# Kernel optimization log

Hardware: AMD Instinct MI355X
Metric: run time of the kernel (lower is better)

Reference implementation:

```python
import jax, jax.numpy as jnp
import numpy as np

N, DIM = 20000, 2
E2, E3 = 150000, 100000
H = 512
IN_PAIR = 2 * DIM + 2    # arity*dim + arity (sigma repeated per object)
IN_TRIPLE = 3 * DIM + 3


def _lin(k, fan_in, fan_out):
    return jax.random.normal(k, (fan_in, fan_out), jnp.float32) / np.sqrt(fan_in)


def setup_inputs() -> dict:
    key = jax.random.key(0)
    ks = jax.random.split(key, 18)
    inp = {
        "x": jax.random.normal(ks[0], (N, DIM), jnp.float32),
        "sigma": jax.random.uniform(ks[1], (1,), jnp.float32) + 0.1,
        "edges_pair": jax.random.randint(ks[2], (E2, 2), 0, N),
        "edges_triple": jax.random.randint(ks[3], (E3, 3), 0, N),
        # per-relation-type TimeInputEnergyMLP params (2 hidden layers + scalar head)
        "pW1": _lin(ks[4], IN_PAIR, H), "pb1": jnp.zeros((H,), jnp.float32),
        "pW2": _lin(ks[5], H, H),       "pb2": jnp.zeros((H,), jnp.float32),
        "pW3": _lin(ks[6], H, 1),       "pb3": jnp.zeros((1,), jnp.float32),
        "tW1": _lin(ks[7], IN_TRIPLE, H), "tb1": jnp.zeros((H,), jnp.float32),
        "tW2": _lin(ks[8], H, H),         "tb2": jnp.zeros((H,), jnp.float32),
        "tW3": _lin(ks[9], H, 1),         "tb3": jnp.zeros((1,), jnp.float32),
    }
    return inp


def _mlp_energy(h, W1, b1, W2, b2, W3, b3):
    # h: (E, in_dim) -> (E, 1) scalar energy per edge
    h = jax.nn.silu(h @ W1 + b1)
    h = jax.nn.silu(h @ W2 + b2)
    return h @ W3 + b3


def reference(x, sigma, edges_pair, edges_triple,
              pW1, pb1, pW2, pb2, pW3, pb3,
              tW1, tb1, tW2, tb2, tW3, tb3):
    def total_energy(xx):
        # pair edges: gather -> (E2, 2*DIM), sigma repeated per object -> (E2, 2)
        xp = xx[edges_pair].reshape(edges_pair.shape[0], -1)
        sp = jnp.broadcast_to(sigma, (edges_pair.shape[0], 2))
        ep = _mlp_energy(jnp.concatenate([xp, sp], axis=-1),
                         pW1, pb1, pW2, pb2, pW3, pb3).sum()
        # triple edges
        xt = xx[edges_triple].reshape(edges_triple.shape[0], -1)
        st = jnp.broadcast_to(sigma, (edges_triple.shape[0], 3))
        et = _mlp_energy(jnp.concatenate([xt, st], axis=-1),
                         tW1, tb1, tW2, tb2, tW3, tb3).sum()
        return ep + et

    energy, grad = jax.value_and_grad(total_energy)(x)
    return energy, grad
```

## Files before the change

kernel.cpp:

```cpp
#include <hip/hip_runtime.h>
#include <hip/hip_bf16.h>

#define HDIM 512
#define TILE 64
#define TPB 512

typedef __attribute__((ext_vector_type(8))) short short8;
typedef __attribute__((ext_vector_type(4))) short s16x4;
typedef __attribute__((ext_vector_type(4))) float f32x4;

__device__ __forceinline__ unsigned short f2bf(float x) {
  __hip_bfloat16 h = __float2bfloat16(x);
  return *reinterpret_cast<unsigned short*>(&h);
}
__device__ __forceinline__ float bf2f(unsigned short h) {
  return __uint_as_float(((unsigned)h) << 16);
}
__device__ __forceinline__ float fsig(float z) {
  return __builtin_amdgcn_rcpf(1.f + __expf(-z));
}
__device__ __forceinline__ int bidx(int e, int n) {
  return e * HDIM + (n ^ ((e & 15) << 3));
}

__global__ void prep_weights(const float* __restrict__ pW2, const float* __restrict__ tW2,
                             unsigned short* __restrict__ pWf, unsigned short* __restrict__ pWb,
                             unsigned short* __restrict__ tWf, unsigned short* __restrict__ tWb) {
  int i = blockIdx.x * blockDim.x + threadIdx.x;
  if (i >= HDIM * HDIM) return;
  int j  = i & 7;
  int l  = (i >> 3) & 63;
  int kb = (i >> 9) & 15;
  int nb = i >> 13;
  int kpos = kb * 32 + ((l >> 4) << 3) + j;
  int npos = nb * 16 + (l & 15);
  pWf[i] = f2bf(pW2[kpos * HDIM + npos]);
  pWb[i] = f2bf(pW2[npos * HDIM + kpos]);
  tWf[i] = f2bf(tW2[kpos * HDIM + npos]);
  tWb[i] = f2bf(tW2[npos * HDIM + kpos]);
}

__global__ void prep_w1(const float* __restrict__ W1, int IN, int GD,
                        unsigned short* __restrict__ hi, unsigned short* __restrict__ lo,
                        unsigned short* __restrict__ p5) {
  int i = blockIdx.x * blockDim.x + threadIdx.x;
  if (i < 32 * 64 * 8) {
    int j = i & 7, l = (i >> 3) & 63, nb = i >> 9;
    int k = ((l >> 4) << 3) + j;
    int col = nb * 16 + (l & 15);
    float v = (k < IN) ? W1[k * HDIM + col] : 0.f;
    unsigned short h = f2bf(v);
    hi[i] = h;
    lo[i] = f2bf(v - bf2f(h));
  } else if (i < 32 * 64 * 8 + 16 * 64 * 8) {
    int i2 = i - 32 * 64 * 8;
    int j = i2 & 7, l = (i2 >> 3) & 63, kk = i2 >> 9;
    int lm = l & 15, q = l >> 4;
    int k = kk * 32 + q * 8 + j;
    p5[i2] = f2bf((lm < GD) ? W1[lm * HDIM + k] : 0.f);
  }
}

__global__ void __launch_bounds__(TPB, 2)
energy_kernel(const float* __restrict__ x, const float* __restrict__ sigp,
              const int* __restrict__ ep, const int* __restrict__ et,
              int E2, int E3, int nb2,
              const unsigned short* __restrict__ pW1hi, const unsigned short* __restrict__ pW1lo,
              const unsigned short* __restrict__ pW1p5,
              const unsigned short* __restrict__ tW1hi, const unsigned short* __restrict__ tW1lo,
              const unsigned short* __restrict__ tW1p5,
              const float* __restrict__ pb1, const float* __restrict__ tb1,
              const unsigned short* __restrict__ pWf, const unsigned short* __restrict__ pWb,
              const unsigned short* __restrict__ tWf, const unsigned short* __restrict__ tWb,
              const float* __restrict__ pb2, const float* __restrict__ tb2,
              const float* __restrict__ pw3, const float* __restrict__ tw3,
              const float* __restrict__ pb3, const float* __restrict__ tb3,
              float* __restrict__ out) {
  __shared__ __align__(16) unsigned short bufA[TILE * HDIM];
  __shared__ __align__(16) float h0s[TILE][16];
  __shared__ float dh0sT[8][TILE];
  __shared__ int   idxs[TILE * 3];
  __shared__ float blockE;

  const bool isP = (int)blockIdx.x < nb2;
  const int arity = isP ? 2 : 3;
  const int GD = 2 * arity;
  const int Etot = isP ? E2 : E3;
  const int* __restrict__ edges = isP ? ep : et;
  const unsigned short* __restrict__ W1hi = isP ? pW1hi : tW1hi;
  const unsigned short* __restrict__ W1lo = isP ? pW1lo : tW1lo;
  const unsigned short* __restrict__ W1p5 = isP ? pW1p5 : tW1p5;
  const unsigned short* __restrict__ Wf = isP ? pWf : tWf;
  const unsigned short* __restrict__ Wb = isP ? pWb : tWb;
  const float* __restrict__ b1 = isP ? pb1 : tb1;
  const float* __restrict__ b2 = isP ? pb2 : tb2;
  const float* __restrict__ w3 = isP ? pw3 : tw3;
  const float* __restrict__ b3p = isP ? pb3 : tb3;

  const int tid  = threadIdx.x;
  const int lane = tid & 63;
  const int w    = tid >> 6;
  const int q    = lane >> 4;
  const int lm   = lane & 15;
  const int tile0 = (isP ? (int)blockIdx.x : (int)blockIdx.x - nb2) * TILE;
  const int vcnt  = min(TILE, Etot - tile0);
  const float sigma = sigp[0];

  if (tid == 0) blockE = 0.f;
  ((float*)dh0sT)[tid] = 0.f;
  if (tid < TILE * arity) {
    int e = tid / arity;
    idxs[tid] = (e < vcnt) ? edges[(size_t)tile0 * arity + tid] : 0;
  }
  __syncthreads();
  if (tid < TILE) {
#pragma unroll
    for (int k = 0; k < 16; ++k) h0s[tid][k] = 0.f;
    if (tid < vcnt) {
      for (int o = 0; o < arity; ++o) {
        int id = idxs[tid * arity + o];
        h0s[tid][o * 2 + 0] = x[id * 2 + 0];
        h0s[tid][o * 2 + 1] = x[id * 2 + 1];
        h0s[tid][arity * 2 + o] = sigma;
      }
    }
  }
  __syncthreads();

  const int n0 = w * 64;

  short8 Hh[4], Hl[4];
#pragma unroll
  for (int ef = 0; ef < 4; ++ef) {
    f32x4 v0 = {0.f, 0.f, 0.f, 0.f}, v1 = {0.f, 0.f, 0.f, 0.f};
    if (q < 2) {
      const float* p = &h0s[ef * 16 + lm][q * 8];
      v0 = *(const f32x4*)p;
      v1 = *(const f32x4*)(p + 4);
    }
#pragma unroll
    for (int j = 0; j < 4; ++j) {
      unsigned short ha = f2bf(v0[j]);
      Hh[ef][j] = (short)ha;
      Hl[ef][j] = (short)f2bf(v0[j] - bf2f(ha));
      unsigned short hb = f2bf(v1[j]);
      Hh[ef][j + 4] = (short)hb;
      Hl[ef][j + 4] = (short)f2bf(v1[j] - bf2f(hb));
    }
  }

  f32x4 acc[4][4];
#pragma unroll
  for (int mf = 0; mf < 4; ++mf)
#pragma unroll
    for (int ef = 0; ef < 4; ++ef) acc[mf][ef] = (f32x4){0.f, 0.f, 0.f, 0.f};

#pragma unroll
  for (int mf = 0; mf < 4; ++mf) {
    short8 A1h = *(const short8*)(W1hi + (((w * 4 + mf) * 64 + lane) << 3));
    short8 A1l = *(const short8*)(W1lo + (((w * 4 + mf) * 64 + lane) << 3));
#pragma unroll
    for (int ef = 0; ef < 4; ++ef) {
      acc[mf][ef] = __builtin_amdgcn_mfma_f32_16x16x32_bf16(A1h, Hh[ef], acc[mf][ef], 0, 0, 0);
      acc[mf][ef] = __builtin_amdgcn_mfma_f32_16x16x32_bf16(A1l, Hh[ef], acc[mf][ef], 0, 0, 0);
      acc[mf][ef] = __builtin_amdgcn_mfma_f32_16x16x32_bf16(A1h, Hl[ef], acc[mf][ef], 0, 0, 0);
    }
  }
#pragma unroll
  for (int mf = 0; mf < 4; ++mf) {
    f32x4 b1x = *(const f32x4*)&b1[n0 + mf * 16 + q * 4];
#pragma unroll
    for (int ef = 0; ef < 4; ++ef) {
      bool val = (ef * 16 + lm) < vcnt;
      s16x4 pk;
#pragma unroll
      for (int r = 0; r < 4; ++r) {
        float z = acc[mf][ef][r] + b1x[r];
        float s = fsig(z);
        pk[r] = (short)f2bf(val ? z * s : 0.f);
      }
      *(s16x4*)&bufA[bidx(ef * 16 + lm, n0 + mf * 16 + q * 4)] = pk;
    }
  }
  __syncthreads();

#pragma unroll
  for (int mf = 0; mf < 4; ++mf)
#pragma unroll
    for (int ef = 0; ef < 4; ++ef) acc[mf][ef] = (f32x4){0.f, 0.f, 0.f, 0.f};

  {
    short8 af_cur[4];
#pragma unroll
    for (int mf = 0; mf < 4; ++mf)
      af_cur[mf] = *(const short8*)(Wf + ((((w * 4 + mf) * 16 + 0) * 64 + lane) << 3));
#pragma unroll
    for (int kk = 0; kk < 16; ++kk) {
      short8 af_nxt[4];
      int kn = (kk + 1) & 15;
#pragma unroll
      for (int mf = 0; mf < 4; ++mf)
        af_nxt[mf] = *(const short8*)(Wf + ((((w * 4 + mf) * 16 + kn) * 64 + lane) << 3));
      short8 hb[4];
#pragma unroll
      for (int ef = 0; ef < 4; ++ef)
        hb[ef] = *(const short8*)&bufA[bidx(ef * 16 + lm, kk * 32 + q * 8)];
      __builtin_amdgcn_s_setprio(1);
#pragma unroll
      for (int mf = 0; mf < 4; ++mf)
#pragma unroll
        for (int ef = 0; ef < 4; ++ef)
          acc[mf][ef] = __builtin_amdgcn_mfma_f32_16x16x32_bf16(af_cur[mf], hb[ef], acc[mf][ef], 0, 0, 0);
      __builtin_amdgcn_s_setprio(0);
#pragma unroll
      for (int mf = 0; mf < 4; ++mf) af_cur[mf] = af_nxt[mf];
    }
  }

  float epart = 0.f;
#pragma unroll
  for (int mf = 0; mf < 4; ++mf) {
    f32x4 b2x = *(const f32x4*)&b2[n0 + mf * 16 + q * 4];
    f32x4 w3x = *(const f32x4*)&w3[n0 + mf * 16 + q * 4];
#pragma unroll
    for (int ef = 0; ef < 4; ++ef) {
      bool val = (ef * 16 + lm) < vcnt;
#pragma unroll
      for (int r = 0; r < 4; ++r) {
        float z = acc[mf][ef][r] + b2x[r];
        float s = fsig(z);
        float h2 = z * s;
        float sp = s * (1.f + z * (1.f - s));
        epart += val ? h2 * w3x[r] : 0.f;
        acc[mf][ef][r] = val ? w3x[r] * sp : 0.f;
      }
    }
  }

  __syncthreads();
#pragma unroll
  for (int mf = 0; mf < 4; ++mf)
#pragma unroll
    for (int ef = 0; ef < 4; ++ef) {
      s16x4 pk;
#pragma unroll
      for (int r = 0; r < 4; ++r) pk[r] = (short)f2bf(acc[mf][ef][r]);
      *(s16x4*)&bufA[bidx(ef * 16 + lm, n0 + mf * 16 + q * 4)] = pk;
    }
#pragma unroll
  for (int off = 32; off > 0; off >>= 1) epart += __shfl_down(epart, off, 64);
  if (lane == 0) atomicAdd(&blockE, epart);
  __syncthreads();
  if (tid == 0) atomicAdd(out, blockE + (float)vcnt * b3p[0]);

#pragma unroll
  for (int mf = 0; mf < 4; ++mf)
#pragma unroll
    for (int ef = 0; ef < 4; ++ef) acc[mf][ef] = (f32x4){0.f, 0.f, 0.f, 0.f};

  {
    short8 af_cur[4];
#pragma unroll
    for (int mf = 0; mf < 4; ++mf)
      af_cur[mf] = *(const short8*)(Wb + ((((w * 4 + mf) * 16 + 0) * 64 + lane) << 3));
#pragma unroll
    for (int kk = 0; kk < 16; ++kk) {
      short8 af_nxt[4];
      int kn = (kk + 1) & 15;
#pragma unroll
      for (int mf = 0; mf < 4; ++mf)
        af_nxt[mf] = *(const short8*)(Wb + ((((w * 4 + mf) * 16 + kn) * 64 + lane) << 3));
      short8 hb[4];
#pragma unroll
      for (int ef = 0; ef < 4; ++ef)
        hb[ef] = *(const short8*)&bufA[bidx(ef * 16 + lm, kk * 32 + q * 8)];
      __builtin_amdgcn_s_setprio(1);
#pragma unroll
      for (int mf = 0; mf < 4; ++mf)
#pragma unroll
        for (int ef = 0; ef < 4; ++ef)
          acc[mf][ef] = __builtin_amdgcn_mfma_f32_16x16x32_bf16(af_cur[mf], hb[ef], acc[mf][ef], 0, 0, 0);
      __builtin_amdgcn_s_setprio(0);
#pragma unroll
      for (int mf = 0; mf < 4; ++mf) af_cur[mf] = af_nxt[mf];
    }
  }

#pragma unroll
  for (int mf = 0; mf < 4; ++mf) {
    short8 A1h = *(const short8*)(W1hi + (((w * 4 + mf) * 64 + lane) << 3));
    f32x4 zacc[4];
#pragma unroll
    for (int ef = 0; ef < 4; ++ef) zacc[ef] = (f32x4){0.f, 0.f, 0.f, 0.f};
#pragma unroll
    for (int ef = 0; ef < 4; ++ef)
      zacc[ef] = __builtin_amdgcn_mfma_f32_16x16x32_bf16(A1h, Hh[ef], zacc[ef], 0, 0, 0);
    f32x4 b1x = *(const f32x4*)&b1[n0 + mf * 16 + q * 4];
#pragma unroll
    for (int ef = 0; ef < 4; ++ef)
#pragma unroll
      for (int r = 0; r < 4; ++r) {
        float z = zacc[ef][r] + b1x[r];
        float s = fsig(z);
        float sp = s * (1.f + z * (1.f - s));
        acc[mf][ef][r] *= sp;
      }
  }
  __syncthreads();
#pragma unroll
  for (int mf = 0; mf < 4; ++mf)
#pragma unroll
    for (int ef = 0; ef < 4; ++ef) {
      s16x4 pk;
#pragma unroll
      for (int r = 0; r < 4; ++r) pk[r] = (short)f2bf(acc[mf][ef][r]);
      *(s16x4*)&bufA[bidx(ef * 16 + lm, n0 + mf * 16 + q * 4)] = pk;
    }
  __syncthreads();

  {
    f32x4 pacc[4];
#pragma unroll
    for (int ef = 0; ef < 4; ++ef) pacc[ef] = (f32x4){0.f, 0.f, 0.f, 0.f};
#pragma unroll
    for (int t = 0; t < 2; ++t) {
      int kk = w * 2 + t;
      short8 a5 = *(const short8*)(W1p5 + ((kk * 64 + lane) << 3));
      short8 db[4];
#pragma unroll
      for (int ef = 0; ef < 4; ++ef)
        db[ef] = *(const short8*)&bufA[bidx(ef * 16 + lm, kk * 32 + q * 8)];
#pragma unroll
      for (int ef = 0; ef < 4; ++ef)
        pacc[ef] = __builtin_amdgcn_mfma_f32_16x16x32_bf16(a5, db[ef], pacc[ef], 0, 0, 0);
    }
#pragma unroll
    for (int ef = 0; ef < 4; ++ef)
#pragma unroll
      for (int r = 0; r < 4; ++r) {
        int g = q * 4 + r;
        if (g < GD) atomicAdd(&dh0sT[g][ef * 16 + lm], pacc[ef][r]);
      }
  }
  __syncthreads();

  {
    int e = tid & 63, g = tid >> 6;
    if (e < vcnt && g < GD) {
      int obj = g >> 1, d = g & 1;
      atomicAdd(&out[1 + idxs[e * arity + obj] * 2 + d], dh0sT[g][e]);
    }
  }
}

extern "C" void kernel_launch(void* const* d_in, const int* in_sizes, int n_in,
                              void* d_out, int out_size, void* d_ws, size_t ws_size,
                              hipStream_t stream) {
  const float* x    = (const float*)d_in[0];
  const float* sig  = (const float*)d_in[1];
  const int*   ep   = (const int*)d_in[2];
  const int*   et   = (const int*)d_in[3];
  const float* pW1  = (const float*)d_in[4];
  const float* pb1  = (const float*)d_in[5];
  const float* pW2  = (const float*)d_in[6];
  const float* pb2  = (const float*)d_in[7];
  const float* pW3  = (const float*)d_in[8];
  const float* pb3  = (const float*)d_in[9];
  const float* tW1  = (const float*)d_in[10];
  const float* tb1  = (const float*)d_in[11];
  const float* tW2  = (const float*)d_in[12];
  const float* tb2  = (const float*)d_in[13];
  const float* tW3  = (const float*)d_in[14];
  const float* tb3  = (const float*)d_in[15];
  const int E2 = in_sizes[2] / 2;
  const int E3 = in_sizes[3] / 3;
  float* out = (float*)d_out;

  unsigned short* pWf = (unsigned short*)d_ws;
  unsigned short* pWb = pWf + HDIM * HDIM;
  unsigned short* tWf = pWb + HDIM * HDIM;
  unsigned short* tWb = tWf + HDIM * HDIM;
  unsigned short* pW1hi = tWb + HDIM * HDIM;
  unsigned short* pW1lo = pW1hi + 32 * 64 * 8;
  unsigned short* pW1p5 = pW1lo + 32 * 64 * 8;
  unsigned short* tW1hi = pW1p5 + 16 * 64 * 8;
  unsigned short* tW1lo = tW1hi + 32 * 64 * 8;
  unsigned short* tW1p5 = tW1lo + 32 * 64 * 8;

  const int nb2 = (E2 + TILE - 1) / TILE;
  const int nb3 = (E3 + TILE - 1) / TILE;

  hipMemsetAsync(d_out, 0, (size_t)out_size * sizeof(float), stream);
  prep_weights<<<(HDIM * HDIM + 255) / 256, 256, 0, stream>>>(pW2, tW2, pWf, pWb, tWf, tWb);
  prep_w1<<<(32 * 64 * 8 + 16 * 64 * 8 + 255) / 256, 256, 0, stream>>>(pW1, 6, 4, pW1hi, pW1lo, pW1p5);
  prep_w1<<<(32 * 64 * 8 + 16 * 64 * 8 + 255) / 256, 256, 0, stream>>>(tW1, 9, 6, tW1hi, tW1lo, tW1p5);
  energy_kernel<<<nb2 + nb3, TPB, 0, stream>>>(
      x, sig, ep, et, E2, E3, nb2,
      pW1hi, pW1lo, pW1p5, tW1hi, tW1lo, tW1p5, pb1, tb1,
      pWf, pWb, tWf, tWb, pb2, tb2, pW3, tW3, pb3, tb3, out);
}
```

Before: 437.3 us.

## Switch MFMA tiling from 16x16x32 to 32x32x16 bf16 instructions

Reworks every matrix stage of the fused energy/gradient kernel (layer-1 split-precision product, forward and backward 512x512 layers, input-gradient projection) to use 32x32x16 MFMA tiles instead of 16x16x32. Weight pre-swizzle kernels and workspace offsets are re-laid out to match the new fragment layout. Larger MFMA tiles mean fewer instructions and more operand reuse per LDS and global fragment load. The cost is more accumulator registers per wave (four f32x16 instead of sixteen f32x4 blocks is the same count, but the epilogue indexing changes) and possible LDS bank-conflict differences under the existing swizzle.

```diff
diff --git a/kernel.cpp b/kernel.cpp
--- a/kernel.cpp
+++ b/kernel.cpp
@@ -8,6 +8,7 @@
 typedef __attribute__((ext_vector_type(8))) short short8;
 typedef __attribute__((ext_vector_type(4))) short s16x4;
 typedef __attribute__((ext_vector_type(4))) float f32x4;
+typedef __attribute__((ext_vector_type(16))) float f32x16;
 
 __device__ __forceinline__ unsigned short f2bf(float x) {
   __hip_bfloat16 h = __float2bfloat16(x);
@@ -30,10 +31,10 @@
   if (i >= HDIM * HDIM) return;
   int j  = i & 7;
   int l  = (i >> 3) & 63;
-  int kb = (i >> 9) & 15;
-  int nb = i >> 13;
-  int kpos = kb * 32 + ((l >> 4) << 3) + j;
-  int npos = nb * 16 + (l & 15);
+  int kc = (i >> 9) & 31;
+  int nb = i >> 14;
+  int npos = nb * 32 + (l & 31);
+  int kpos = kc * 16 + ((l >> 5) << 3) + j;
   pWf[i] = f2bf(pW2[kpos * HDIM + npos]);
   pWb[i] = f2bf(pW2[npos * HDIM + kpos]);
   tWf[i] = f2bf(tW2[kpos * HDIM + npos]);
@@ -44,20 +45,20 @@
                         unsigned short* __restrict__ hi, unsigned short* __restrict__ lo,
                         unsigned short* __restrict__ p5) {
   int i = blockIdx.x * blockDim.x + threadIdx.x;
-  if (i < 32 * 64 * 8) {
+  if (i < 16 * 64 * 8) {
     int j = i & 7, l = (i >> 3) & 63, nb = i >> 9;
-    int k = ((l >> 4) << 3) + j;
-    int col = nb * 16 + (l & 15);
+    int k = ((l >> 5) << 3) + j;
+    int col = nb * 32 + (l & 31);
     float v = (k < IN) ? W1[k * HDIM + col] : 0.f;
     unsigned short h = f2bf(v);
     hi[i] = h;
     lo[i] = f2bf(v - bf2f(h));
-  } else if (i < 32 * 64 * 8 + 16 * 64 * 8) {
-    int i2 = i - 32 * 64 * 8;
-    int j = i2 & 7, l = (i2 >> 3) & 63, kk = i2 >> 9;
-    int lm = l & 15, q = l >> 4;
-    int k = kk * 32 + q * 8 + j;
-    p5[i2] = f2bf((lm < GD) ? W1[lm * HDIM + k] : 0.f);
+  } else if (i < 16 * 64 * 8 + 32 * 64 * 8) {
+    int i2 = i - 16 * 64 * 8;
+    int j = i2 & 7, l = (i2 >> 3) & 63, kc = i2 >> 9;
+    int g = l & 31;
+    int n = kc * 16 + ((l >> 5) << 3) + j;
+    p5[i2] = f2bf((g < GD) ? W1[g * HDIM + n] : 0.f);
   }
 }
 
@@ -100,8 +101,8 @@
   const int tid  = threadIdx.x;
   const int lane = tid & 63;
   const int w    = tid >> 6;
-  const int q    = lane >> 4;
-  const int lm   = lane & 15;
+  const int l31  = lane & 31;
+  const int lh   = lane >> 5;
   const int tile0 = (isP ? (int)blockIdx.x : (int)blockIdx.x - nb2) * TILE;
   const int vcnt  = min(TILE, Etot - tile0);
   const float sigma = sigp[0];
@@ -129,124 +130,155 @@
 
   const int n0 = w * 64;
 
-  short8 Hh[4], Hl[4];
-#pragma unroll
-  for (int ef = 0; ef < 4; ++ef) {
-    f32x4 v0 = {0.f, 0.f, 0.f, 0.f}, v1 = {0.f, 0.f, 0.f, 0.f};
-    if (q < 2) {
-      const float* p = &h0s[ef * 16 + lm][q * 8];
-      v0 = *(const f32x4*)p;
-      v1 = *(const f32x4*)(p + 4);
-    }
-#pragma unroll
-    for (int j = 0; j < 4; ++j) {
-      unsigned short ha = f2bf(v0[j]);
-      Hh[ef][j] = (short)ha;
-      Hl[ef][j] = (short)f2bf(v0[j] - bf2f(ha));
-      unsigned short hb = f2bf(v1[j]);
-      Hh[ef][j + 4] = (short)hb;
-      Hl[ef][j + 4] = (short)f2bf(v1[j] - bf2f(hb));
-    }
-  }
-
-  f32x4 acc[4][4];
-#pragma unroll
-  for (int mf = 0; mf < 4; ++mf)
-#pragma unroll
-    for (int ef = 0; ef < 4; ++ef) acc[mf][ef] = (f32x4){0.f, 0.f, 0.f, 0.f};
-
-#pragma unroll
-  for (int mf = 0; mf < 4; ++mf) {
-    short8 A1h = *(const short8*)(W1hi + (((w * 4 + mf) * 64 + lane) << 3));
-    short8 A1l = *(const short8*)(W1lo + (((w * 4 + mf) * 64 + lane) << 3));
-#pragma unroll
-    for (int ef = 0; ef < 4; ++ef) {
-      acc[mf][ef] = __builtin_amdgcn_mfma_f32_16x16x32_bf16(A1h, Hh[ef], acc[mf][ef], 0, 0, 0);
-      acc[mf][ef] = __builtin_amdgcn_mfma_f32_16x16x32_bf16(A1l, Hh[ef], acc[mf][ef], 0, 0, 0);
-      acc[mf][ef] = __builtin_amdgcn_mfma_f32_16x16x32_bf16(A1h, Hl[ef], acc[mf][ef], 0, 0, 0);
-    }
-  }
-#pragma unroll
-  for (int mf = 0; mf < 4; ++mf) {
-    f32x4 b1x = *(const f32x4*)&b1[n0 + mf * 16 + q * 4];
-#pragma unroll
-    for (int ef = 0; ef < 4; ++ef) {
-      bool val = (ef * 16 + lm) < vcnt;
-      s16x4 pk;
-#pragma unroll
-      for (int r = 0; r < 4; ++r) {
-        float z = acc[mf][ef][r] + b1x[r];
-        float s = fsig(z);
-        pk[r] = (short)f2bf(val ? z * s : 0.f);
-      }
-      *(s16x4*)&bufA[bidx(ef * 16 + lm, n0 + mf * 16 + q * 4)] = pk;
-    }
-  }
-  __syncthreads();
-
-#pragma unroll
-  for (int mf = 0; mf < 4; ++mf)
-#pragma unroll
-    for (int ef = 0; ef < 4; ++ef) acc[mf][ef] = (f32x4){0.f, 0.f, 0.f, 0.f};
-
+  short8 Hh[2];
+  f32x16 acc[2][2];
   {
-    short8 af_cur[4];
-#pragma unroll
-    for (int mf = 0; mf < 4; ++mf)
-      af_cur[mf] = *(const short8*)(Wf + ((((w * 4 + mf) * 16 + 0) * 64 + lane) << 3));
-#pragma unroll
-    for (int kk = 0; kk < 16; ++kk) {
-      short8 af_nxt[4];
-      int kn = (kk + 1) & 15;
-#pragma unroll
-      for (int mf = 0; mf < 4; ++mf)
-        af_nxt[mf] = *(const short8*)(Wf + ((((w * 4 + mf) * 16 + kn) * 64 + lane) << 3));
-      short8 hb[4];
-#pragma unroll
-      for (int ef = 0; ef < 4; ++ef)
-        hb[ef] = *(const short8*)&bufA[bidx(ef * 16 + lm, kk * 32 + q * 8)];
+    short8 Hl[2];
+#pragma unroll
+    for (int eb = 0; eb < 2; ++eb) {
+      const float* p = &h0s[eb * 32 + l31][lh * 8];
+      f32x4 v0 = *(const f32x4*)p;
+      f32x4 v1 = *(const f32x4*)(p + 4);
+#pragma unroll
+      for (int j = 0; j < 4; ++j) {
+        unsigned short ha = f2bf(v0[j]);
+        Hh[eb][j] = (short)ha;
+        Hl[eb][j] = (short)f2bf(v0[j] - bf2f(ha));
+        unsigned short hb_ = f2bf(v1[j]);
+        Hh[eb][j + 4] = (short)hb_;
+        Hl[eb][j + 4] = (short)f2bf(v1[j] - bf2f(hb_));
+      }
+    }
+#pragma unroll
+    for (int nb = 0; nb < 2; ++nb)
+#pragma unroll
+      for (int eb = 0; eb < 2; ++eb)
+#pragma unroll
+        for (int r = 0; r < 16; ++r) acc[nb][eb][r] = 0.f;
+
+#pragma unroll
+    for (int nb = 0; nb < 2; ++nb) {
+      int nbg = w * 2 + nb;
+      short8 A1h = *(const short8*)(W1hi + ((nbg * 64 + lane) << 3));
+      short8 A1l = *(const short8*)(W1lo + ((nbg * 64 + lane) << 3));
+#pragma unroll
+      for (int eb = 0; eb < 2; ++eb) {
+        acc[nb][eb] = __builtin_amdgcn_mfma_f32_32x32x16_bf16(A1h, Hh[eb], acc[nb][eb], 0, 0, 0);
+        acc[nb][eb] = __builtin_amdgcn_mfma_f32_32x32x16_bf16(A1l, Hh[eb], acc[nb][eb], 0, 0, 0);
+        acc[nb][eb] = __builtin_amdgcn_mfma_f32_32x32x16_bf16(A1h, Hl[eb], acc[nb][eb], 0, 0, 0);
+      }
+    }
+  }
+#pragma unroll
+  for (int nb = 0; nb < 2; ++nb) {
+    int nbase = n0 + nb * 32;
+#pragma unroll
+    for (int eb = 0; eb < 2; ++eb) {
+      int e = eb * 32 + l31;
+      bool val = e < vcnt;
+#pragma unroll
+      for (int g = 0; g < 4; ++g) {
+        int n4 = nbase + 8 * g + 4 * lh;
+        f32x4 b1x = *(const f32x4*)&b1[n4];
+        s16x4 pk;
+#pragma unroll
+        for (int r = 0; r < 4; ++r) {
+          float z = acc[nb][eb][4 * g + r] + b1x[r];
+          float s = fsig(z);
+          pk[r] = (short)f2bf(val ? z * s : 0.f);
+        }
+        *(s16x4*)&bufA[bidx(e, n4)] = pk;
+      }
+    }
+  }
+  __syncthreads();
+
+#pragma unroll
+  for (int nb = 0; nb < 2; ++nb)
+#pragma unroll
+    for (int eb = 0; eb < 2; ++eb)
+#pragma unroll
+      for (int r = 0; r < 16; ++r) acc[nb][eb][r] = 0.f;
+
+  {
+    short8 af_cur[2][2];
+#pragma unroll
+    for (int nb = 0; nb < 2; ++nb)
+#pragma unroll
+      for (int t = 0; t < 2; ++t)
+        af_cur[nb][t] = *(const short8*)(Wf + ((((w * 2 + nb) * 32 + t) * 64 + lane) << 3));
+#pragma unroll
+    for (int c = 0; c < 16; ++c) {
+      short8 af_nxt[2][2];
+      int cn = (c + 1) & 15;
+#pragma unroll
+      for (int nb = 0; nb < 2; ++nb)
+#pragma unroll
+        for (int t = 0; t < 2; ++t)
+          af_nxt[nb][t] = *(const short8*)(Wf + ((((w * 2 + nb) * 32 + cn * 2 + t) * 64 + lane) << 3));
+      short8 hb[2][2];
+#pragma unroll
+      for (int eb = 0; eb < 2; ++eb)
+#pragma unroll
+        for (int t = 0; t < 2; ++t)
+          hb[eb][t] = *(const short8*)&bufA[bidx(eb * 32 + l31, (c * 2 + t) * 16 + lh * 8)];
       __builtin_amdgcn_s_setprio(1);
 #pragma unroll
-      for (int mf = 0; mf < 4; ++mf)
-#pragma unroll
-        for (int ef = 0; ef < 4; ++ef)
-          acc[mf][ef] = __builtin_amdgcn_mfma_f32_16x16x32_bf16(af_cur[mf], hb[ef], acc[mf][ef], 0, 0, 0);
+      for (int t = 0; t < 2; ++t)
+#pragma unroll
+        for (int nb = 0; nb < 2; ++nb)
+#pragma unroll
+          for (int eb = 0; eb < 2; ++eb)
+            acc[nb][eb] = __builtin_amdgcn_mfma_f32_32x32x16_bf16(af_cur[nb][t], hb[eb][t], acc[nb][eb], 0, 0, 0);
       __builtin_amdgcn_s_setprio(0);
 #pragma unroll
-      for (int mf = 0; mf < 4; ++mf) af_cur[mf] = af_nxt[mf];
+      for (int nb = 0; nb < 2; ++nb)
+#pragma unroll
+        for (int t = 0; t < 2; ++t) af_cur[nb][t] = af_nxt[nb][t];
     }
   }
 
   float epart = 0.f;
 #pragma unroll
-  for (int mf = 0; mf < 4; ++mf) {
-    f32x4 b2x = *(const f32x4*)&b2[n0 + mf * 16 + q * 4];
-    f32x4 w3x = *(const f32x4*)&w3[n0 + mf * 16 + q * 4];
-#pragma unroll
-    for (int ef = 0; ef < 4; ++ef) {
-      bool val = (ef * 16 + lm) < vcnt;
-#pragma unroll
-      for (int r = 0; r < 4; ++r) {
-        float z = acc[mf][ef][r] + b2x[r];
-        float s = fsig(z);
-        float h2 = z * s;
-        float sp = s * (1.f + z * (1.f - s));
-        epart += val ? h2 * w3x[r] : 0.f;
-        acc[mf][ef][r] = val ? w3x[r] * sp : 0.f;
-      }
-    }
-  }
-
-  __syncthreads();
-#pragma unroll
-  for (int mf = 0; mf < 4; ++mf)
-#pragma unroll
-    for (int ef = 0; ef < 4; ++ef) {
-      s16x4 pk;
-#pragma unroll
-      for (int r = 0; r < 4; ++r) pk[r] = (short)f2bf(acc[mf][ef][r]);
-      *(s16x4*)&bufA[bidx(ef * 16 + lm, n0 + mf * 16 + q * 4)] = pk;
-    }
+  for (int nb = 0; nb < 2; ++nb) {
+    int nbase = n0 + nb * 32;
+#pragma unroll
+    for (int eb = 0; eb < 2; ++eb) {
+      bool val = (eb * 32 + l31) < vcnt;
+#pragma unroll
+      for (int g = 0; g < 4; ++g) {
+        int n4 = nbase + 8 * g + 4 * lh;
+        f32x4 b2x = *(const f32x4*)&b2[n4];
+        f32x4 w3x = *(const f32x4*)&w3[n4];
+#pragma unroll
+        for (int r = 0; r < 4; ++r) {
+          float z = acc[nb][eb][4 * g + r] + b2x[r];
+          float s = fsig(z);
+          float h2 = z * s;
+          float sp = s * (1.f + z * (1.f - s));
+          epart += val ? h2 * w3x[r] : 0.f;
+          acc[nb][eb][4 * g + r] = val ? w3x[r] * sp : 0.f;
+        }
+      }
+    }
+  }
+
+  __syncthreads();
+#pragma unroll
+  for (int nb = 0; nb < 2; ++nb) {
+    int nbase = n0 + nb * 32;
+#pragma unroll
+    for (int eb = 0; eb < 2; ++eb) {
+      int e = eb * 32 + l31;
+#pragma unroll
+      for (int g = 0; g < 4; ++g) {
+        s16x4 pk;
+#pragma unroll
+        for (int r = 0; r < 4; ++r) pk[r] = (short)f2bf(acc[nb][eb][4 * g + r]);
+        *(s16x4*)&bufA[bidx(e, nbase + 8 * g + 4 * lh)] = pk;
+      }
+    }
+  }
 #pragma unroll
   for (int off = 32; off > 0; off >>= 1) epart += __shfl_down(epart, off, 64);
   if (lane == 0) atomicAdd(&blockE, epart);
@@ -254,92 +286,114 @@
   if (tid == 0) atomicAdd(out, blockE + (float)vcnt * b3p[0]);
 
 #pragma unroll
-  for (int mf = 0; mf < 4; ++mf)
-#pragma unroll
-    for (int ef = 0; ef < 4; ++ef) acc[mf][ef] = (f32x4){0.f, 0.f, 0.f, 0.f};
+  for (int nb = 0; nb < 2; ++nb)
+#pragma unroll
+    for (int eb = 0; eb < 2; ++eb)
+#pragma unroll
+      for (int r = 0; r < 16; ++r) acc[nb][eb][r] = 0.f;
 
   {
-    short8 af_cur[4];
-#pragma unroll
-    for (int mf = 0; mf < 4; ++mf)
-      af_cur[mf] = *(const short8*)(Wb + ((((w * 4 + mf) * 16 + 0) * 64 + lane) << 3));
-#pragma unroll
-    for (int kk = 0; kk < 16; ++kk) {
-      short8 af_nxt[4];
-      int kn = (kk + 1) & 15;
-#pragma unroll
-      for (int mf = 0; mf < 4; ++mf)
-        af_nxt[mf] = *(const short8*)(Wb + ((((w * 4 + mf) * 16 + kn) * 64 + lane) << 3));
-      short8 hb[4];
-#pragma unroll
-      for (int ef = 0; ef < 4; ++ef)
-        hb[ef] = *(const short8*)&bufA[bidx(ef * 16 + lm, kk * 32 + q * 8)];
+    short8 af_cur[2][2];
+#pragma unroll
+    for (int nb = 0; nb < 2; ++nb)
+#pragma unroll
+      for (int t = 0; t < 2; ++t)
+        af_cur[nb][t] = *(const short8*)(Wb + ((((w * 2 + nb) * 32 + t) * 64 + lane) << 3));
+#pragma unroll
+    for (int c = 0; c < 16; ++c) {
+      short8 af_nxt[2][2];
+      int cn = (c + 1) & 15;
+#pragma unroll
+      for (int nb = 0; nb < 2; ++nb)
+#pragma unroll
+        for (int t = 0; t < 2; ++t)
+          af_nxt[nb][t] = *(const short8*)(Wb + ((((w * 2 + nb) * 32 + cn * 2 + t) * 64 + lane) << 3));
+      short8 hb[2][2];
+#pragma unroll
+      for (int eb = 0; eb < 2; ++eb)
+#pragma unroll
+        for (int t = 0; t < 2; ++t)
+          hb[eb][t] = *(const short8*)&bufA[bidx(eb * 32 + l31, (c * 2 + t) * 16 + lh * 8)];
       __builtin_amdgcn_s_setprio(1);
 #pragma unroll
-      for (int mf = 0; mf < 4; ++mf)
-#pragma unroll
-        for (int ef = 0; ef < 4; ++ef)
-          acc[mf][ef] = __builtin_amdgcn_mfma_f32_16x16x32_bf16(af_cur[mf], hb[ef], acc[mf][ef], 0, 0, 0);
+      for (int t = 0; t < 2; ++t)
+#pragma unroll
+        for (int nb = 0; nb < 2; ++nb)
+#pragma unroll
+          for (int eb = 0; eb < 2; ++eb)
+            acc[nb][eb] = __builtin_amdgcn_mfma_f32_32x32x16_bf16(af_cur[nb][t], hb[eb][t], acc[nb][eb], 0, 0, 0);
       __builtin_amdgcn_s_setprio(0);
 #pragma unroll
-      for (int mf = 0; mf < 4; ++mf) af_cur[mf] = af_nxt[mf];
-    }
-  }
-
-#pragma unroll
-  for (int mf = 0; mf < 4; ++mf) {
-    short8 A1h = *(const short8*)(W1hi + (((w * 4 + mf) * 64 + lane) << 3));
-    f32x4 zacc[4];
-#pragma unroll
-    for (int ef = 0; ef < 4; ++ef) zacc[ef] = (f32x4){0.f, 0.f, 0.f, 0.f};
-#pragma unroll
-    for (int ef = 0; ef < 4; ++ef)
-      zacc[ef] = __builtin_amdgcn_mfma_f32_16x16x32_bf16(A1h, Hh[ef], zacc[ef], 0, 0, 0);
-    f32x4 b1x = *(const f32x4*)&b1[n0 + mf * 16 + q * 4];
-#pragma unroll
-    for (int ef = 0; ef < 4; ++ef)
+      for (int nb = 0; nb < 2; ++nb)
+#pragma unroll
+        for (int t = 0; t < 2; ++t) af_cur[nb][t] = af_nxt[nb][t];
+    }
+  }
+
+#pragma unroll
+  for (int nb = 0; nb < 2; ++nb) {
+    int nbg = w * 2 + nb;
+    int nbase = n0 + nb * 32;
+    short8 A1h = *(const short8*)(W1hi + ((nbg * 64 + lane) << 3));
+#pragma unroll
+    for (int eb = 0; eb < 2; ++eb) {
+      f32x16 zacc;
+#pragma unroll
+      for (int r = 0; r < 16; ++r) zacc[r] = 0.f;
+      zacc = __builtin_amdgcn_mfma_f32_32x32x16_bf16(A1h, Hh[eb], zacc, 0, 0, 0);
+#pragma unroll
+      for (int g = 0; g < 4; ++g) {
+        f32x4 b1x = *(const f32x4*)&b1[nbase + 8 * g + 4 * lh];
+#pragma unroll
+        for (int r = 0; r < 4; ++r) {
+          float z = zacc[4 * g + r] + b1x[r];
+          float s = fsig(z);
+          float sp = s * (1.f + z * (1.f - s));
+          acc[nb][eb][4 * g + r] *= sp;
+        }
+      }
+    }
+  }
+  __syncthreads();
+#pragma unroll
+  for (int nb = 0; nb < 2; ++nb) {
+    int nbase = n0 + nb * 32;
+#pragma unroll
+    for (int eb = 0; eb < 2; ++eb) {
+      int e = eb * 32 + l31;
+#pragma unroll
+      for (int g = 0; g < 4; ++g) {
+        s16x4 pk;
+#pragma unroll
+        for (int r = 0; r < 4; ++r) pk[r] = (short)f2bf(acc[nb][eb][4 * g + r]);
+        *(s16x4*)&bufA[bidx(e, nbase + 8 * g + 4 * lh)] = pk;
+      }
+    }
+  }
+  __syncthreads();
+
+  {
+    f32x16 pacc[2];
+#pragma unroll
+    for (int eb = 0; eb < 2; ++eb)
+#pragma unroll
+      for (int r = 0; r < 16; ++r) pacc[eb][r] = 0.f;
+#pragma unroll
+    for (int t = 0; t < 4; ++t) {
+      int kc = w * 4 + t;
+      short8 a5 = *(const short8*)(W1p5 + ((kc * 64 + lane) << 3));
+#pragma unroll
+      for (int eb = 0; eb < 2; ++eb) {
+        short8 db = *(const short8*)&bufA[bidx(eb * 32 + l31, kc * 16 + lh * 8)];
+        pacc[eb] = __builtin_amdgcn_mfma_f32_32x32x16_bf16(a5, db, pacc[eb], 0, 0, 0);
+      }
+    }
+#pragma unroll
+    for (int eb = 0; eb < 2; ++eb)
 #pragma unroll
       for (int r = 0; r < 4; ++r) {
-        float z = zacc[ef][r] + b1x[r];
-        float s = fsig(z);
-        float sp = s * (1.f + z * (1.f - s));
-        acc[mf][ef][r] *= sp;
-      }
-  }
-  __syncthreads();
-#pragma unroll
-  for (int mf = 0; mf < 4; ++mf)
-#pragma unroll
-    for (int ef = 0; ef < 4; ++ef) {
-      s16x4 pk;
-#pragma unroll
-      for (int r = 0; r < 4; ++r) pk[r] = (short)f2bf(acc[mf][ef][r]);
-      *(s16x4*)&bufA[bidx(ef * 16 + lm, n0 + mf * 16 + q * 4)] = pk;
-    }
-  __syncthreads();
-
-  {
-    f32x4 pacc[4];
-#pragma unroll
-    for (int ef = 0; ef < 4; ++ef) pacc[ef] = (f32x4){0.f, 0.f, 0.f, 0.f};
-#pragma unroll
-    for (int t = 0; t < 2; ++t) {
-      int kk = w * 2 + t;
-      short8 a5 = *(const short8*)(W1p5 + ((kk * 64 + lane) << 3));
-      short8 db[4];
-#pragma unroll
-      for (int ef = 0; ef < 4; ++ef)
-        db[ef] = *(const short8*)&bufA[bidx(ef * 16 + lm, kk * 32 + q * 8)];
-#pragma unroll
-      for (int ef = 0; ef < 4; ++ef)
-        pacc[ef] = __builtin_amdgcn_mfma_f32_16x16x32_bf16(a5, db[ef], pacc[ef], 0, 0, 0);
-    }
-#pragma unroll
-    for (int ef = 0; ef < 4; ++ef)
-#pragma unroll
-      for (int r = 0; r < 4; ++r) {
-        int g = q * 4 + r;
-        if (g < GD) atomicAdd(&dh0sT[g][ef * 16 + lm], pacc[ef][r]);
+        int g = r + 4 * lh;
+        if (g < GD) atomicAdd(&dh0sT[g][eb * 32 + l31], pacc[eb][r]);
       }
   }
   __syncthreads();
@@ -381,19 +435,19 @@
   unsigned short* tWf = pWb + HDIM * HDIM;
   unsigned short* tWb = tWf + HDIM * HDIM;
   unsigned short* pW1hi = tWb + HDIM * HDIM;
-  unsigned short* pW1lo = pW1hi + 32 * 64 * 8;
-  unsigned short* pW1p5 = pW1lo + 32 * 64 * 8;
-  unsigned short* tW1hi = pW1p5 + 16 * 64 * 8;
-  unsigned short* tW1lo = tW1hi + 32 * 64 * 8;
-  unsigned short* tW1p5 = tW1lo + 32 * 64 * 8;
+  unsigned short* pW1lo = pW1hi + 16 * 64 * 8;
+  unsigned short* pW1p5 = pW1lo + 16 * 64 * 8;
+  unsigned short* tW1hi = pW1p5 + 32 * 64 * 8;
+  unsigned short* tW1lo = tW1hi + 16 * 64 * 8;
+  unsigned short* tW1p5 = tW1lo + 16 * 64 * 8;
 
   const int nb2 = (E2 + TILE - 1) / TILE;
   const int nb3 = (E3 + TILE - 1) / TILE;
 
   hipMemsetAsync(d_out, 0, (size_t)out_size * sizeof(float), stream);
   prep_weights<<<(HDIM * HDIM + 255) / 256, 256, 0, stream>>>(pW2, tW2, pWf, pWb, tWf, tWb);
-  prep_w1<<<(32 * 64 * 8 + 16 * 64 * 8 + 255) / 256, 256, 0, stream>>>(pW1, 6, 4, pW1hi, pW1lo, pW1p5);
-  prep_w1<<<(32 * 64 * 8 + 16 * 64 * 8 + 255) / 256, 256, 0, stream>>>(tW1, 9, 6, tW1hi, tW1lo, tW1p5);
+  prep_w1<<<(16 * 64 * 8 + 32 * 64 * 8 + 255) / 256, 256, 0, stream>>>(pW1, 6, 4, pW1hi, pW1lo, pW1p5);
+  prep_w1<<<(16 * 64 * 8 + 32 * 64 * 8 + 255) / 256, 256, 0, stream>>>(tW1, 9, 6, tW1hi, tW1lo, tW1p5);
   energy_kernel<<<nb2 + nb3, TPB, 0, stream>>>(
       x, sig, ep, et, E2, E3, nb2,
       pW1hi, pW1lo, pW1p5, tW1hi, tW1lo, tW1p5, pb1, tb1,
```

Measured after the change: 438.8 us. About the same (+0.4%).
